# Optimization experiments

Measured on AMD Instinct MI355X. Metric: run time of the kernel, lower is better.

Reference implementation:

```python
import jax, jax.numpy as jnp
import numpy as np
from jax import lax

BN_EPS = 1e-5
TINY = 1e-12


def conv2d(x, w, stride, padding):
    # NCHW x OIHW -> NCHW
    return lax.conv_general_dilated(
        x, w, (stride, stride), [(padding, padding), (padding, padding)],
        dimension_numbers=('NCHW', 'OIHW', 'NCHW'))


def pool2x2(x):
    B, C, H, W = x.shape
    return x.reshape(B, C, H // 2, 2, W // 2, 2).mean(axis=(3, 5))


def setup_inputs() -> dict:
    key = jax.random.key(0)
    k0, k1, k2, k3 = jax.random.split(key, 4)
    B, Cin, H, W = 32, 128, 56, 56
    Cout, K = 256, 3
    mean = jax.random.normal(k0, (B, Cin, H, W), jnp.float32)
    std = jax.random.uniform(k1, (B, Cin, H, W), jnp.float32)  # std must be >= 0
    fan_in = Cin * K * K
    bound = 1.0 / np.sqrt(fan_in)  # torch Conv2d default init
    conv_w = jax.random.uniform(k2, (Cout, Cin, K, K), jnp.float32, -bound, bound)
    conv_b = jax.random.uniform(k3, (Cout,), jnp.float32, -bound, bound)
    bn_gamma = jnp.full((Cout,), 2.5, jnp.float32)  # module fills weight with 2.5
    bn_beta = jnp.full((Cout,), 2.5, jnp.float32)   # module fills bias with 2.5
    return {'mean': mean, 'std': std, 'conv_w': conv_w, 'conv_b': conv_b,
            'bn_gamma': bn_gamma, 'bn_beta': bn_beta}


def reference(mean, std, conv_w, conv_b, bn_gamma, bn_beta):
    # mean branch: standard conv
    m = conv2d(mean, conv_w, 1, 1) + conv_b[None, :, None, None]
    # std branch (no rho): independent-variance propagation, var -> conv with w^2
    var = conv2d(std * std, conv_w * conv_w, 1, 1)
    s = jnp.sqrt(var + TINY)
    # BatchNorm2d in training mode: batch statistics over (N, H, W)
    mu = jnp.mean(m, axis=(0, 2, 3), keepdims=True)
    v = jnp.var(m, axis=(0, 2, 3), keepdims=True)  # biased, like torch normalization
    inv = 1.0 / jnp.sqrt(v + BN_EPS)
    g = bn_gamma[None, :, None, None]
    uhat = (m - mu) * inv * g + bn_beta[None, :, None, None]
    # std through BN: pure linear scale by |gamma| / sqrt(var + eps)
    shat = s * inv * jnp.abs(g)
    # moment activation (erf-based Gaussian->Heaviside moment mapping)
    z = uhat / (shat * np.sqrt(2.0) + TINY)
    u = 0.5 * (1.0 + lax.erf(z))               # output mean in (0, 1)
    sa = jnp.sqrt(jnp.clip(u * (1.0 - u), TINY))  # output std of Bernoulli-like moments
    # avg-pool 2x2 stride 2: mean pools linearly, independent vars: std = sqrt(avg(var))/2
    u_p = pool2x2(u)
    s_p = jnp.sqrt(pool2x2(sa * sa)) * 0.5
    return (u_p, s_p)
```

## Files before the change

### kernel.cpp

```cpp
#include <hip/hip_runtime.h>
#include <hip/hip_bf16.h>
#include <math.h>

#define BB 32
#define CIN 128
#define HH 56
#define WW 56
#define COUT 256
#define HW (HH*WW)
#define NPIX (BB*HW)
#define PH 28
#define PW 28
#define POOL_ELEMS ((long)BB*COUT*PH*PW)
#define PADH 58
#define PADW 58
#define TRANS_BLOCKS ((BB*PADH*PADW*16)/256)
#define WPACK_BLOCKS ((9*COUT*CIN)/256)

typedef unsigned short u16;
using s16x8 = __attribute__((ext_vector_type(8))) short;
using s16x4 = __attribute__((ext_vector_type(4))) short;
using f32x4 = __attribute__((ext_vector_type(4))) float;

__device__ __forceinline__ float b2f(u16 u){ return __uint_as_float(((unsigned)u)<<16); }
__device__ __forceinline__ u16 f2b(float x){
    unsigned u = __float_as_uint(x);
    unsigned r = (u + 0x7fffu + ((u>>16)&1u)) >> 16;
    return (u16)r;
}

__device__ __forceinline__ void gload16(const void* g, void* l){
    __builtin_amdgcn_global_load_lds(
        (const __attribute__((address_space(1))) unsigned int*)g,
        (__attribute__((address_space(3))) unsigned int*)l, 16, 0, 0);
}


__global__ __launch_bounds__(256) void prep_kernel(
    const float* __restrict__ mean, const float* __restrict__ stdv,
    const float* __restrict__ w,
    u16* __restrict__ mean_pad, u16* __restrict__ std2_pad,
    u16* __restrict__ BP, u16* __restrict__ BP2)
{
    int bid = blockIdx.x;
    if (bid < TRANS_BLOCKS){
        int t   = bid*256 + threadIdx.x;
        int oct = t & 15;
        int pp  = t >> 4;
        int pw = pp % PADW; int tmp = pp / PADW;
        int ph = tmp % PADH; int b = tmp / PADH;
        size_t obase = (size_t)pp*CIN + oct*8;
        s16x8 pm = (s16x8){0,0,0,0,0,0,0,0}, ps = pm;
        if (ph >= 1 && ph <= HH && pw >= 1 && pw <= WW){
            long ibase = ((long)(b*CIN + oct*8)*HH + (ph-1))*WW + (pw-1);
            #pragma unroll
            for (int j=0;j<8;j++){
                float m = mean[ibase + (long)j*HW];
                float s = stdv[ibase + (long)j*HW];
                pm[j] = (short)f2b(m);
                ps[j] = (short)f2b(s*s);
            }
        }
        *(s16x8*)(mean_pad + obase) = pm;
        *(s16x8*)(std2_pad + obase) = ps;
    } else {
        int t = (bid - TRANS_BLOCKS)*256 + threadIdx.x;
        int e    = t & 7;
        int co   = (t >> 3) & 255;
        int rest = t >> 11;
        int ks   = rest >> 2;
        int sub  = rest & 3;
        int r    = ks >> 2;
        int ci   = (ks & 3)*32 + sub*8 + e;
        float v = w[((long)co*CIN + ci)*9 + r];
        BP[t]  = f2b(v);
        BP2[t] = f2b(v*v);
    }
}

__global__ __launch_bounds__(256,2) void convw_kernel(
    const u16* __restrict__ mean_pad, const u16* __restrict__ std2_pad,
    const u16* __restrict__ BP, const u16* __restrict__ BP2,
    const float* __restrict__ bias,
    u16* __restrict__ m_out, u16* __restrict__ v_out,
    float* __restrict__ sum_, float* __restrict__ sumsq_)
{
    __shared__ u16 lds[32768];
    const int tid  = threadIdx.x;
    const int lane = tid & 63;
    const int wv   = tid >> 6;

    int gid   = blockIdx.x;
    int local = gid >> 3;
    int p     = (gid & 7)*112 + (local >> 2);
    int v4    = local & 3;
    int path  = v4 >> 1;
    int co_blk= (v4 & 1) * 128;
    const int b  = p / 28;
    const int h0 = (p - b*28) * 2;

    const u16* __restrict__ Ap = path ? std2_pad : mean_pad;
    const u16* __restrict__ Bp = path ? BP2      : BP;
    u16*       __restrict__ Op = path ? v_out    : m_out;

    const int slot_g = (tid & 15) ^ ((tid >> 4) & 7);
    const int wbase  = (b*PADH + h0)*PADW*CIN;
    const int athr   = (tid >> 4)*CIN + slot_g*8;
    #pragma unroll
    for (int i=0; i<16; ++i){
        const int Ci = (i>>2)*(PADW*CIN) + (i&3)*16*CIN;
        gload16(Ap + wbase + Ci + athr, &lds[i*2048 + tid*8]);
    }
    __syncthreads();

    int R0[7];
    #pragma unroll
    for (int mi=0; mi<7; ++mi){
        int px = mi*16 + (lane & 15);
        int dh = (px >= 56) ? 1 : 0;
        R0[mi] = dh*64 + (px - dh*56);
    }
    const int q = lane >> 4;

    const u16* bp = Bp + (size_t)((lane>>4)*256 + co_blk + wv*32 + (lane&15))*8;

    f32x4 acc[7][2];
    #pragma unroll
    for (int i=0;i<7;i++){ acc[i][0] = (f32x4){0,0,0,0}; acc[i][1] = (f32x4){0,0,0,0}; }

    #pragma unroll
    for (int r=0; r<9; ++r){
        const int kh = r/3, kw = r - (r/3)*3;
        s16x8 bf[2][2][2];
        #pragma unroll
        for (int hf=0; hf<2; ++hf)
          #pragma unroll
          for (int kk=0; kk<2; ++kk)
            #pragma unroll
            for (int ni=0; ni<2; ++ni)
              bf[hf][kk][ni] = *(const s16x8*)(bp + (size_t)(r*4 + hf*2 + kk)*8192 + ni*128);

        int ab[7];
        #pragma unroll
        for (int mi=0; mi<7; ++mi){
            int R  = R0[mi] + kh*64 + kw;
            int t7 = (R0[mi] + kw) & 7;
            ab[mi] = R*128 + ((q ^ t7) << 3);
        }

        #pragma unroll
        for (int hf=0; hf<2; ++hf){
            #pragma unroll
            for (int kk=0; kk<2; ++kk){
                const int off = hf*64, kx = kk*32;
                s16x8 af[7];
                #pragma unroll
                for (int mi=0; mi<7; ++mi)
                    af[mi] = *(const s16x8*)&lds[(ab[mi] + off) ^ kx];
                #pragma unroll
                for (int mi=0; mi<7; ++mi){
                    acc[mi][0] = __builtin_amdgcn_mfma_f32_16x16x32_bf16(af[mi], bf[hf][kk][0], acc[mi][0], 0,0,0);
                    acc[mi][1] = __builtin_amdgcn_mfma_f32_16x16x32_bf16(af[mi], bf[hf][kk][1], acc[mi][1], 0,0,0);
                }
            }
        }
    }

    float bv[2];
    if (path == 0){
        #pragma unroll
        for (int ni=0;ni<2;ni++) bv[ni] = bias[co_blk + wv*32 + ni*16 + (lane&15)];
    } else {
        bv[0] = 0.f; bv[1] = 0.f;
    }

    float ssum[2] = {0.f,0.f}, ssq[2] = {0.f,0.f};

    #pragma unroll
    for (int mi=0; mi<7; ++mi){
        int px = mi*16 + ((lane>>4)<<2);
        int dh = (px >= 56) ? 1 : 0;
        int w  = px - dh*56;
        #pragma unroll
        for (int ni=0; ni<2; ++ni){
            int co = co_blk + wv*32 + ni*16 + (lane&15);
            size_t o = (size_t)(b*COUT + co)*HW + (size_t)(h0+dh)*WW + w;
            s16x4 pk;
            #pragma unroll
            for (int rr=0; rr<4; ++rr){
                float vv = acc[mi][ni][rr] + bv[ni];
                pk[rr] = (short)f2b(vv);
                ssum[ni] += vv;
                ssq[ni]  += vv*vv;
            }
            *(s16x4*)(Op + o) = pk;
        }
    }

    if (path == 0){
        #pragma unroll
        for (int ni=0; ni<2; ++ni){
            float s = ssum[ni], s2 = ssq[ni];
            s  += __shfl_xor(s, 16, 64);  s2 += __shfl_xor(s2, 16, 64);
            s  += __shfl_xor(s, 32, 64);  s2 += __shfl_xor(s2, 32, 64);
            if (lane < 16){
                int co = co_blk + wv*32 + ni*16 + lane;
                atomicAdd(&sum_[co],   s);
                atomicAdd(&sumsq_[co], s2);
            }
        }
    }
}

__global__ __launch_bounds__(256) void final_kernel(
        const u16* __restrict__ m, const u16* __restrict__ var,
        const float* __restrict__ sum_, const float* __restrict__ sumsq_,
        const float* __restrict__ gamma, const float* __restrict__ beta,
        float* __restrict__ out){
    int idx4 = blockIdx.x*256 + threadIdx.x;
    int wo4 = idx4 % (PW/4); int t = idx4 / (PW/4);
    int ho = t % PH; t /= PH;
    int co = t % COUT; int b = t / COUT;
    float g  = gamma[co];
    float be = beta[co];
    float mu = sum_[co] / (float)NPIX;
    float vr = sumsq_[co] / (float)NPIX - mu*mu;
    float inv = 1.0f / sqrtf(vr + 1e-5f);
    float ag = fabsf(g);
    float us[4] = {0.f,0.f,0.f,0.f}, ss[4] = {0.f,0.f,0.f,0.f};
    #pragma unroll
    for (int dh=0; dh<2; ++dh){
        long base = ((long)(b*COUT+co)*HH + 2*ho+dh)*WW + wo4*8;
        const s16x8 vm = *(const s16x8*)&m[base];
        const s16x8 vv = *(const s16x8*)&var[base];
        #pragma unroll
        for (int j=0;j<8;j++){
            float mm = b2f((u16)vm[j]);
            float sdev = sqrtf(b2f((u16)vv[j]) + 1e-12f);
            float uhat = (mm - mu)*inv*g + be;
            float shat = sdev*inv*ag;
            float z = uhat / (shat*1.41421356237f + 1e-12f);
            float u = 0.5f*(1.f + erff(z));
            us[j>>1] += u;
            ss[j>>1] += fmaxf(u*(1.f-u), 1e-12f);
        }
    }
    long ob = ((long)(b*COUT+co)*PH + ho)*PW + wo4*4;
    f32x4 o0, o1;
    #pragma unroll
    for (int k=0;k<4;k++){
        o0[k] = 0.25f*us[k];
        o1[k] = sqrtf(0.25f*ss[k])*0.5f;
    }
    *(f32x4*)(out + ob) = o0;
    *(f32x4*)(out + POOL_ELEMS + ob) = o1;
}


__global__ void wtransf_kernel(const float* __restrict__ w, float* __restrict__ wT){
    int out = blockIdx.x*256 + threadIdx.x;
    if (out >= COUT*CIN*9) return;
    int co = out % COUT;
    int r  = out / COUT;
    wT[out] = w[(long)co*(CIN*9) + r];
}

__global__ __launch_bounds__(256) void stats_old_kernel(const u16* __restrict__ m,
        float* __restrict__ mu_out, float* __restrict__ inv_out){
    int co = blockIdx.x;
    float s=0.f, s2=0.f;
    for (int oc = threadIdx.x; oc < NPIX/8; oc += 256){
        int b = oc / (HW/8); int o8 = oc - b*(HW/8);
        const s16x8 v8 = *(const s16x8*)&m[((size_t)(b*COUT+co))*HW + (size_t)o8*8];
        #pragma unroll
        for (int j=0;j<8;j++){ float v = b2f((u16)v8[j]); s += v; s2 += v*v; }
    }
    __shared__ float rs[256], rs2[256];
    rs[threadIdx.x]=s; rs2[threadIdx.x]=s2; __syncthreads();
    for (int o=128;o>0;o>>=1){
        if (threadIdx.x < o){ rs[threadIdx.x]+=rs[threadIdx.x+o]; rs2[threadIdx.x]+=rs2[threadIdx.x+o]; }
        __syncthreads();
    }
    if (threadIdx.x==0){
        float mu = rs[0]/(float)NPIX;
        float var = rs2[0]/(float)NPIX - mu*mu;
        mu_out[co] = mu;
        inv_out[co] = 1.0f/sqrtf(var + 1e-5f);
    }
}

__global__ __launch_bounds__(256) void final_old_kernel(
        const u16* __restrict__ m, const u16* __restrict__ var,
        const float* __restrict__ mu_, const float* __restrict__ inv_,
        const float* __restrict__ gamma, const float* __restrict__ beta,
        float* __restrict__ out){
    long idx = (long)blockIdx.x*256 + threadIdx.x;
    int wo = (int)(idx % PW); long t = idx / PW;
    int ho = (int)(t % PH); t /= PH;
    int co = (int)(t % COUT); int b = (int)(t / COUT);
    float g  = gamma[co];
    float be = beta[co];
    float mu = mu_[co], inv = inv_[co];
    float ag = fabsf(g);
    float us = 0.f, ss = 0.f;
    #pragma unroll
    for (int dh=0; dh<2; ++dh){
        int hpos = 2*ho+dh;
        long base = ((long)(b*COUT+co)*HH + hpos)*WW + 2*wo;
        #pragma unroll
        for (int dw=0; dw<2; ++dw){
            float mm = b2f(m[base+dw]);
            float vv = b2f(var[base+dw]);
            float sdev = sqrtf(vv + 1e-12f);
            float uhat = (mm - mu)*inv*g + be;
            float shat = sdev*inv*ag;
            float z = uhat / (shat*1.41421356237f + 1e-12f);
            float u = 0.5f*(1.f + erff(z));
            float sa2 = fmaxf(u*(1.f-u), 1e-12f);
            us += u; ss += sa2;
        }
    }
    out[idx]              = 0.25f*us;
    out[POOL_ELEMS + idx] = sqrtf(0.25f*ss)*0.5f;
}

#define CI_CHUNK 64
#define XW 32
__global__ __launch_bounds__(256) void conv_old_kernel(
    const float* __restrict__ mean, const float* __restrict__ stdv,
    const float* __restrict__ wT, const float* __restrict__ bias,
    u16* __restrict__ m_out, u16* __restrict__ v_out)
{
    __shared__ float lds_m[CI_CHUNK][3][XW];
    __shared__ float lds_s[CI_CHUNK][3][XW];
    const int co   = threadIdx.x;
    const int half = blockIdx.x;
    const int h    = blockIdx.y;
    const int b    = blockIdx.z;
    const int w_base = half*28;

    float acc_m[28], acc_v[28];
    #pragma unroll
    for (int i=0;i<28;i++){ acc_m[i]=0.f; acc_v[i]=0.f; }

    for (int c=0; c<CIN; c+=CI_CHUNK){
        for (int t = threadIdx.x; t < CI_CHUNK*3*30; t += 256){
            int pos = t % 30; int r = t / 30; int hh = r % 3; int ci_l = r / 3;
            int gh = h - 1 + hh; int gw = w_base - 1 + pos;
            float vm = 0.f, vs = 0.f;
            if ((unsigned)gh < (unsigned)HH && (unsigned)gw < (unsigned)WW){
                long gi = ((long)(b*CIN + (c+ci_l))*HH + gh)*WW + gw;
                vm = mean[gi];
                float sv = stdv[gi];
                vs = sv*sv;
            }
            lds_m[ci_l][hh][pos] = vm;
            lds_s[ci_l][hh][pos] = vs;
        }
        __syncthreads();
        for (int ci_l=0; ci_l<CI_CHUNK; ++ci_l){
            int rbase = (c+ci_l)*9;
            #pragma unroll
            for (int kh=0; kh<3; ++kh){
                float w0 = wT[(long)(rbase + kh*3 + 0)*COUT + co];
                float w1 = wT[(long)(rbase + kh*3 + 1)*COUT + co];
                float w2 = wT[(long)(rbase + kh*3 + 2)*COUT + co];
                float xm[30];
                #pragma unroll
                for (int p=0;p<30;p++) xm[p] = lds_m[ci_l][kh][p];
                #pragma unroll
                for (int i=0;i<28;i++) acc_m[i] += w0*xm[i] + w1*xm[i+1] + w2*xm[i+2];
                float q0=w0*w0, q1=w1*w1, q2=w2*w2;
                float xs[30];
                #pragma unroll
                for (int p=0;p<30;p++) xs[p] = lds_s[ci_l][kh][p];
                #pragma unroll
                for (int i=0;i<28;i++) acc_v[i] += q0*xs[i] + q1*xs[i+1] + q2*xs[i+2];
            }
        }
        __syncthreads();
    }
    float bvv = bias[co];
    long obase = ((long)(b*COUT+co)*HH + h)*WW + w_base;
    #pragma unroll
    for (int i=0;i<28;i++){
        m_out[obase+i] = f2b(acc_m[i]+bvv);
        v_out[obase+i] = f2b(acc_v[i]);
    }
}

extern "C" void kernel_launch(void* const* d_in, const int* in_sizes, int n_in,
                              void* d_out, int out_size, void* d_ws, size_t ws_size,
                              hipStream_t stream)
{
    const float* mean   = (const float*)d_in[0];
    const float* stdv   = (const float*)d_in[1];
    const float* conv_w = (const float*)d_in[2];
    const float* conv_b = (const float*)d_in[3];
    const float* gamma  = (const float*)d_in[4];
    const float* beta   = (const float*)d_in[5];
    float* out = (float*)d_out;
    char* ws = (char*)d_ws;

    const size_t PAD_BYTES  = (size_t)BB*PADH*PADW*CIN*2;
    const size_t SLACK      = 8192;
    const size_t OFF_STD2   = PAD_BYTES + SLACK;
    const size_t OFF_WT     = OFF_STD2 + PAD_BYTES + SLACK;
    const size_t WT_BYTES   = (size_t)9*COUT*CIN*2;
    const size_t OFF_WT2    = OFF_WT + WT_BYTES;
    const size_t OFF_M      = OFF_WT2 + WT_BYTES;
    const size_t MV_BYTES   = (size_t)BB*COUT*HW*2;
    const size_t OFF_V      = OFF_M + MV_BYTES;
    const size_t OFF_SUM    = OFF_V + MV_BYTES;
    const size_t OFF_SUMSQ  = OFF_SUM + 1024;
    const size_t NEED_FAST  = OFF_SUMSQ + 1024;

    if (ws_size >= NEED_FAST){
        u16* mean_pad = (u16*)ws;
        u16* std2_pad = (u16*)(ws + OFF_STD2);
        u16* BP   = (u16*)(ws + OFF_WT);
        u16* BP2  = (u16*)(ws + OFF_WT2);
        u16* m_buf = (u16*)(ws + OFF_M);
        u16* v_buf = (u16*)(ws + OFF_V);
        float* sum_   = (float*)(ws + OFF_SUM);
        float* sumsq_ = (float*)(ws + OFF_SUMSQ);

        hipMemsetAsync(ws + OFF_SUM, 0, 2048, stream);
        prep_kernel<<<TRANS_BLOCKS + WPACK_BLOCKS, 256, 0, stream>>>(
            mean, stdv, conv_w, mean_pad, std2_pad, BP, BP2);
        convw_kernel<<<(NPIX/112)*2*2, 256, 0, stream>>>(
            mean_pad, std2_pad, BP, BP2, conv_b, m_buf, v_buf, sum_, sumsq_);
        final_kernel<<<(int)(POOL_ELEMS/4/256), 256, 0, stream>>>(
            m_buf, v_buf, sum_, sumsq_, gamma, beta, out);
    } else {
        u16* m_buf = (u16*)ws;
        u16* v_buf = (u16*)(ws + (size_t)BB*COUT*HW*2);
        float* wT  = (float*)(ws + (size_t)BB*COUT*HW*4);
        float* mu  = (float*)(ws + (size_t)BB*COUT*HW*4 + (size_t)COUT*CIN*9*4);
        float* inv = mu + 256;
        wtransf_kernel<<<(COUT*CIN*9+255)/256, 256, 0, stream>>>(conv_w, wT);
        conv_old_kernel<<<dim3(2, HH, BB), 256, 0, stream>>>(mean, stdv, wT, conv_b, m_buf, v_buf);
        stats_old_kernel<<<COUT, 256, 0, stream>>>(m_buf, mu, inv);
        final_old_kernel<<<(int)(POOL_ELEMS/256), 256, 0, stream>>>(m_buf, v_buf, mu, inv, gamma, beta, out);
    }
}
```

Measured before the change: 236.5 us.

## Widen conv block tile to all 256 output channels, halving block count

Each conv block now computes all 256 output channels for its 112-pixel tile instead of splitting them across two blocks. This halves the LDS staging of the input window per output and halves the grid size. B fragments are now loaded inside the inner k-loop rather than preloaded per tap. Accumulators double to 7x4 f32x4 per thread, which raises register pressure under launch_bounds(256,2) and may cause spills or lower occupancy.

```diff
diff --git a/kernel.cpp b/kernel.cpp
--- a/kernel.cpp
+++ b/kernel.cpp
@@ -92,10 +92,8 @@
 
     int gid   = blockIdx.x;
     int local = gid >> 3;
-    int p     = (gid & 7)*112 + (local >> 2);
-    int v4    = local & 3;
-    int path  = v4 >> 1;
-    int co_blk= (v4 & 1) * 128;
+    int p     = (gid & 7)*112 + (local >> 1);
+    int path  = local & 1;
     const int b  = p / 28;
     const int h0 = (p - b*28) * 2;
 
@@ -122,23 +120,17 @@
     }
     const int q = lane >> 4;
 
-    const u16* bp = Bp + (size_t)((lane>>4)*256 + co_blk + wv*32 + (lane&15))*8;
-
-    f32x4 acc[7][2];
-    #pragma unroll
-    for (int i=0;i<7;i++){ acc[i][0] = (f32x4){0,0,0,0}; acc[i][1] = (f32x4){0,0,0,0}; }
+    const u16* bp = Bp + (size_t)((lane>>4)*256 + wv*64 + (lane&15))*8;
+
+    f32x4 acc[7][4];
+    #pragma unroll
+    for (int i=0;i<7;i++)
+      #pragma unroll
+      for (int j=0;j<4;j++) acc[i][j] = (f32x4){0,0,0,0};
 
     #pragma unroll
     for (int r=0; r<9; ++r){
         const int kh = r/3, kw = r - (r/3)*3;
-        s16x8 bf[2][2][2];
-        #pragma unroll
-        for (int hf=0; hf<2; ++hf)
-          #pragma unroll
-          for (int kk=0; kk<2; ++kk)
-            #pragma unroll
-            for (int ni=0; ni<2; ++ni)
-              bf[hf][kk][ni] = *(const s16x8*)(bp + (size_t)(r*4 + hf*2 + kk)*8192 + ni*128);
 
         int ab[7];
         #pragma unroll
@@ -152,6 +144,11 @@
         for (int hf=0; hf<2; ++hf){
             #pragma unroll
             for (int kk=0; kk<2; ++kk){
+                const size_t ksoff = (size_t)(r*4 + hf*2 + kk)*8192;
+                s16x8 bf0 = *(const s16x8*)(bp + ksoff);
+                s16x8 bf1 = *(const s16x8*)(bp + ksoff + 128);
+                s16x8 bf2 = *(const s16x8*)(bp + ksoff + 256);
+                s16x8 bf3 = *(const s16x8*)(bp + ksoff + 384);
                 const int off = hf*64, kx = kk*32;
                 s16x8 af[7];
                 #pragma unroll
@@ -159,22 +156,25 @@
                     af[mi] = *(const s16x8*)&lds[(ab[mi] + off) ^ kx];
                 #pragma unroll
                 for (int mi=0; mi<7; ++mi){
-                    acc[mi][0] = __builtin_amdgcn_mfma_f32_16x16x32_bf16(af[mi], bf[hf][kk][0], acc[mi][0], 0,0,0);
-                    acc[mi][1] = __builtin_amdgcn_mfma_f32_16x16x32_bf16(af[mi], bf[hf][kk][1], acc[mi][1], 0,0,0);
+                    acc[mi][0] = __builtin_amdgcn_mfma_f32_16x16x32_bf16(af[mi], bf0, acc[mi][0], 0,0,0);
+                    acc[mi][1] = __builtin_amdgcn_mfma_f32_16x16x32_bf16(af[mi], bf1, acc[mi][1], 0,0,0);
+                    acc[mi][2] = __builtin_amdgcn_mfma_f32_16x16x32_bf16(af[mi], bf2, acc[mi][2], 0,0,0);
+                    acc[mi][3] = __builtin_amdgcn_mfma_f32_16x16x32_bf16(af[mi], bf3, acc[mi][3], 0,0,0);
                 }
             }
         }
     }
 
-    float bv[2];
+    float bv[4];
     if (path == 0){
         #pragma unroll
-        for (int ni=0;ni<2;ni++) bv[ni] = bias[co_blk + wv*32 + ni*16 + (lane&15)];
+        for (int ni=0;ni<4;ni++) bv[ni] = bias[wv*64 + ni*16 + (lane&15)];
     } else {
-        bv[0] = 0.f; bv[1] = 0.f;
-    }
-
-    float ssum[2] = {0.f,0.f}, ssq[2] = {0.f,0.f};
+        #pragma unroll
+        for (int ni=0;ni<4;ni++) bv[ni] = 0.f;
+    }
+
+    float ssum[4] = {0.f,0.f,0.f,0.f}, ssq[4] = {0.f,0.f,0.f,0.f};
 
     #pragma unroll
     for (int mi=0; mi<7; ++mi){
@@ -182,8 +182,8 @@
         int dh = (px >= 56) ? 1 : 0;
         int w  = px - dh*56;
         #pragma unroll
-        for (int ni=0; ni<2; ++ni){
-            int co = co_blk + wv*32 + ni*16 + (lane&15);
+        for (int ni=0; ni<4; ++ni){
+            int co = wv*64 + ni*16 + (lane&15);
             size_t o = (size_t)(b*COUT + co)*HW + (size_t)(h0+dh)*WW + w;
             s16x4 pk;
             #pragma unroll
@@ -199,12 +199,12 @@
 
     if (path == 0){
         #pragma unroll
-        for (int ni=0; ni<2; ++ni){
+        for (int ni=0; ni<4; ++ni){
             float s = ssum[ni], s2 = ssq[ni];
             s  += __shfl_xor(s, 16, 64);  s2 += __shfl_xor(s2, 16, 64);
             s  += __shfl_xor(s, 32, 64);  s2 += __shfl_xor(s2, 32, 64);
             if (lane < 16){
-                int co = co_blk + wv*32 + ni*16 + lane;
+                int co = wv*64 + ni*16 + lane;
                 atomicAdd(&sum_[co],   s);
                 atomicAdd(&sumsq_[co], s2);
             }
@@ -428,7 +428,7 @@
         hipMemsetAsync(ws + OFF_SUM, 0, 2048, stream);
         prep_kernel<<<TRANS_BLOCKS + WPACK_BLOCKS, 256, 0, stream>>>(
             mean, stdv, conv_w, mean_pad, std2_pad, BP, BP2);
-        convw_kernel<<<(NPIX/112)*2*2, 256, 0, stream>>>(
+        convw_kernel<<<(NPIX/112)*2, 256, 0, stream>>>(
             mean_pad, std2_pad, BP, BP2, conv_b, m_buf, v_buf, sum_, sumsq_);
         final_kernel<<<(int)(POOL_ELEMS/4/256), 256, 0, stream>>>(
             m_buf, v_buf, sum_, sumsq_, gamma, beta, out);
```

Result: faster. 230.1 us (-2.7%).

## Split conv input-channel loop into two LDS halves to raise occupancy

Applied to the files above, without the earlier changes.

The conv kernel now stages only 64 of the 128 input channels in shared memory at a time, looping over two channel halves with a barrier between them. This halves LDS use to 32KB and lowers register pressure by loading fewer weight fragments per tap, so the launch bound goes from 2 to 3 blocks per SIMD. The cost is a second global-to-LDS load phase with extra synchronisation that cannot overlap with compute, and the swizzle pattern changes to match the narrower rows.

```diff
diff --git a/kernel.cpp b/kernel.cpp
--- a/kernel.cpp
+++ b/kernel.cpp
@@ -78,14 +78,14 @@
     }
 }
 
-__global__ __launch_bounds__(256,2) void convw_kernel(
+__global__ __launch_bounds__(256,3) void convw_kernel(
     const u16* __restrict__ mean_pad, const u16* __restrict__ std2_pad,
     const u16* __restrict__ BP, const u16* __restrict__ BP2,
     const float* __restrict__ bias,
     u16* __restrict__ m_out, u16* __restrict__ v_out,
     float* __restrict__ sum_, float* __restrict__ sumsq_)
 {
-    __shared__ u16 lds[32768];
+    __shared__ u16 lds[16384];
     const int tid  = threadIdx.x;
     const int lane = tid & 63;
     const int wv   = tid >> 6;
@@ -103,15 +103,9 @@
     const u16* __restrict__ Bp = path ? BP2      : BP;
     u16*       __restrict__ Op = path ? v_out    : m_out;
 
-    const int slot_g = (tid & 15) ^ ((tid >> 4) & 7);
+    const int slot_g = (tid & 7) ^ ((tid >> 3) & 7);
     const int wbase  = (b*PADH + h0)*PADW*CIN;
-    const int athr   = (tid >> 4)*CIN + slot_g*8;
-    #pragma unroll
-    for (int i=0; i<16; ++i){
-        const int Ci = (i>>2)*(PADW*CIN) + (i&3)*16*CIN;
-        gload16(Ap + wbase + Ci + athr, &lds[i*2048 + tid*8]);
-    }
-    __syncthreads();
+    const int off0   = (tid >> 3)*CIN + slot_g*8;
 
     int R0[7];
     #pragma unroll
@@ -120,47 +114,50 @@
         int dh = (px >= 56) ? 1 : 0;
         R0[mi] = dh*64 + (px - dh*56);
     }
-    const int q = lane >> 4;
-
-    const u16* bp = Bp + (size_t)((lane>>4)*256 + co_blk + wv*32 + (lane&15))*8;
+    const int g = lane >> 4;
+
+    const u16* bp = Bp + (size_t)(g*256 + co_blk + wv*32 + (lane&15))*8;
 
     f32x4 acc[7][2];
     #pragma unroll
     for (int i=0;i<7;i++){ acc[i][0] = (f32x4){0,0,0,0}; acc[i][1] = (f32x4){0,0,0,0}; }
 
     #pragma unroll
-    for (int r=0; r<9; ++r){
-        const int kh = r/3, kw = r - (r/3)*3;
-        s16x8 bf[2][2][2];
-        #pragma unroll
-        for (int hf=0; hf<2; ++hf)
-          #pragma unroll
-          for (int kk=0; kk<2; ++kk)
-            #pragma unroll
-            for (int ni=0; ni<2; ++ni)
-              bf[hf][kk][ni] = *(const s16x8*)(bp + (size_t)(r*4 + hf*2 + kk)*8192 + ni*128);
-
-        int ab[7];
-        #pragma unroll
-        for (int mi=0; mi<7; ++mi){
-            int R  = R0[mi] + kh*64 + kw;
-            int t7 = (R0[mi] + kw) & 7;
-            ab[mi] = R*128 + ((q ^ t7) << 3);
-        }
-
-        #pragma unroll
-        for (int hf=0; hf<2; ++hf){
+    for (int H=0; H<2; ++H){
+        if (H) __syncthreads();
+        {
+            const u16* src0 = Ap + wbase + off0 + H*64;
+            #pragma unroll
+            for (int i=0; i<8; ++i){
+                gload16(src0 + (i>>1)*(PADW*CIN) + (i&1)*(32*CIN), &lds[i*2048 + tid*8]);
+            }
+        }
+        __syncthreads();
+
+        #pragma unroll
+        for (int r=0; r<9; ++r){
+            const int kh = r/3, kw = r - (r/3)*3;
+            int ab[7];
+            #pragma unroll
+            for (int mi=0; mi<7; ++mi){
+                int R  = R0[mi] + kh*64 + kw;
+                int t7 = (R0[mi] + kw) & 7;
+                ab[mi] = R*64 + ((g ^ t7) << 3);
+            }
             #pragma unroll
             for (int kk=0; kk<2; ++kk){
-                const int off = hf*64, kx = kk*32;
+                const size_t ksoff = (size_t)(r*4 + H*2 + kk)*8192;
+                s16x8 bf0 = *(const s16x8*)(bp + ksoff);
+                s16x8 bf1 = *(const s16x8*)(bp + ksoff + 128);
+                const int kx = kk*32;
                 s16x8 af[7];
                 #pragma unroll
                 for (int mi=0; mi<7; ++mi)
-                    af[mi] = *(const s16x8*)&lds[(ab[mi] + off) ^ kx];
+                    af[mi] = *(const s16x8*)&lds[ab[mi] ^ kx];
                 #pragma unroll
                 for (int mi=0; mi<7; ++mi){
-                    acc[mi][0] = __builtin_amdgcn_mfma_f32_16x16x32_bf16(af[mi], bf[hf][kk][0], acc[mi][0], 0,0,0);
-                    acc[mi][1] = __builtin_amdgcn_mfma_f32_16x16x32_bf16(af[mi], bf[hf][kk][1], acc[mi][1], 0,0,0);
+                    acc[mi][0] = __builtin_amdgcn_mfma_f32_16x16x32_bf16(af[mi], bf0, acc[mi][0], 0,0,0);
+                    acc[mi][1] = __builtin_amdgcn_mfma_f32_16x16x32_bf16(af[mi], bf1, acc[mi][1], 0,0,0);
                 }
             }
         }
@@ -168,8 +165,8 @@
 
     float bv[2];
     if (path == 0){
-        #pragma unroll
-        for (int ni=0;ni<2;ni++) bv[ni] = bias[co_blk + wv*32 + ni*16 + (lane&15)];
+        bv[0] = bias[co_blk + wv*32 + (lane&15)];
+        bv[1] = bias[co_blk + wv*32 + 16 + (lane&15)];
     } else {
         bv[0] = 0.f; bv[1] = 0.f;
     }
```

Result: slower. 278.4 us (+17.7%).
